# Performance work log

Measured on AMD Instinct MI355X. Metric: run time of the kernel, lower is better.

The kernel has to match this reference:

```python
import jax, jax.numpy as jnp
import numpy as np

D = 256          # input_size
RNN = 256        # rnn_hidden
COND = 64        # cond_dim
HID = 128        # MLP hidden
N_FIXED = 128    # mask.sum() with alternating mask
N_FREE = D - N_FIXED
B = 131072

# Static index arrays implementing the boolean mask (even indices fixed).
IDX_FIXED = np.arange(0, D, 2)
IDX_FREE = np.arange(1, D, 2)


def setup_inputs() -> dict:
    key = jax.random.key(0)
    ks = jax.random.split(key, 8)
    in_dim = N_FIXED + RNN + COND  # 448
    x = jax.random.normal(ks[0], (B, D), jnp.float32)
    h = jax.random.normal(ks[1], (B, RNN + COND), jnp.float32)
    W1 = jax.random.normal(ks[2], (in_dim, HID), jnp.float32) / np.sqrt(in_dim)
    b1 = jnp.zeros((HID,), jnp.float32)
    W2 = jax.random.normal(ks[3], (HID, HID), jnp.float32) / np.sqrt(HID)
    b2 = jnp.zeros((HID,), jnp.float32)
    W3 = jax.random.normal(ks[4], (HID, N_FREE * 2), jnp.float32) / np.sqrt(HID)
    b3 = jnp.zeros((N_FREE * 2,), jnp.float32)
    return {"x": x, "h": h, "W1": W1, "b1": b1, "W2": W2, "b2": b2, "W3": W3, "b3": b3}


def reference(x, h, W1, b1, W2, b2, W3, b3):
    # gather fixed / free halves (static index gather == boolean-mask select)
    x_fixed = x[:, IDX_FIXED]          # [B, N_FIXED]
    x_free = x[:, IDX_FREE]            # [B, N_FREE]
    z = jnp.concatenate([x_fixed, h], axis=-1)  # [B, 448]
    a = jax.nn.relu(z @ W1 + b1)
    a = jax.nn.relu(a @ W2 + b2)
    st = a @ W3 + b3                   # [B, 2*N_FREE]
    s = jnp.tanh(st[:, :N_FREE])
    t = st[:, N_FREE:]
    y_free = x_free * jnp.exp(s) + t
    log_det = jnp.sum(s, axis=-1)
    # scatter-write back into output layout
    y = jnp.zeros_like(x).at[:, IDX_FIXED].set(x_fixed).at[:, IDX_FREE].set(y_free)
    return y, log_det
```

## Files before the change

kernel.cpp:

```cpp
#include <hip/hip_runtime.h>
#include <stdint.h>

typedef __attribute__((ext_vector_type(8))) short bf16x8;
typedef __attribute__((ext_vector_type(4))) float f32x4;

#define B_ROWS 131072
#define BM 32
#define ZP 456
#define AP 136

#define Z_OFF    0
#define Z_BYTES  (BM * ZP * 2)
#define A1_OFF   (Z_OFF + Z_BYTES)
#define A1_BYTES (BM * AP * 2)
#define BIAS_OFF (A1_OFF + A1_BYTES)
#define BIAS_BYTES (512 * 4)
#define LDET_OFF (BIAS_OFF + BIAS_BYTES)
#define LDS_TOTAL (LDET_OFF + 4 * BM * 4)

#define W1P_OFF 0
#define W2P_OFF 7168
#define W3P_OFF 9216

__device__ inline uint16_t f2bf(float x) {
  uint32_t u = __float_as_uint(x);
  u += 0x7fffu + ((u >> 16) & 1u);
  return (uint16_t)(u >> 16);
}

__device__ inline float tanh_fast(float x) {
  x = fminf(fmaxf(x, -15.f), 15.f);
  float e = __expf(2.f * x);
  return (e - 1.f) / (e + 1.f);
}

__global__ void prepack_kernel(const float* __restrict__ W1,
                               const float* __restrict__ W2,
                               const float* __restrict__ W3,
                               uint4* __restrict__ wp) {
  int tid = blockIdx.x * 256 + threadIdx.x;
  if (tid >= 13312) return;
  int l = tid & 63, f = tid >> 6;
  const float* W; int N, kt, nt;
  if (f < 112)      { W = W1; N = 128; int ff = f;       nt = ff / 14; kt = ff - nt * 14; }
  else if (f < 144) { W = W2; N = 128; int ff = f - 112; nt = ff >> 2; kt = ff & 3; }
  else              { W = W3; N = 256; int ff = f - 144; nt = ff >> 2; kt = ff & 3; }
  int k0  = kt * 32 + (l >> 4) * 8;
  int col = nt * 16 + (l & 15);
  uint16_t v[8];
#pragma unroll
  for (int j = 0; j < 8; j++) v[j] = f2bf(W[(size_t)(k0 + j) * N + col]);
  uint4 o;
  o.x = (uint32_t)v[0] | ((uint32_t)v[1] << 16);
  o.y = (uint32_t)v[2] | ((uint32_t)v[3] << 16);
  o.z = (uint32_t)v[4] | ((uint32_t)v[5] << 16);
  o.w = (uint32_t)v[6] | ((uint32_t)v[7] << 16);
  wp[tid] = o;
}

__global__ __launch_bounds__(256, 4) void fused_kernel(
    const float* __restrict__ x, const float* __restrict__ h,
    const float* __restrict__ b1, const float* __restrict__ b2,
    const float* __restrict__ b3, const uint4* __restrict__ wp,
    float* __restrict__ y, float* __restrict__ ldet) {
  extern __shared__ uint8_t smem[];
  uint16_t* zs  = (uint16_t*)(smem + Z_OFF);
  uint16_t* a1  = (uint16_t*)(smem + A1_OFF);
  uint16_t* a2  = (uint16_t*)(smem + Z_OFF);
  float*    bias = (float*)(smem + BIAS_OFF);
  float*    lsum = (float*)(smem + LDET_OFF);

  const int t  = threadIdx.x;
  const int m0 = blockIdx.x * BM;

  for (int i = t; i < 512; i += 256)
    bias[i] = (i < 128) ? b1[i] : (i < 256) ? b2[i - 128] : b3[i - 256];

  {
    const float4* xg = (const float4*)(x + (size_t)m0 * 256);
#pragma unroll
    for (int k = 0; k < 8; k++) {
      int idx = t + k * 256;
      int row = idx >> 6, c4 = idx & 63;
      float4 v = xg[idx];
      uint32_t p = (uint32_t)f2bf(v.x) | ((uint32_t)f2bf(v.z) << 16);
      *(uint32_t*)&zs[row * ZP + c4 * 2] = p;
    }
    const float4* hg = (const float4*)(h + (size_t)m0 * 320);
#pragma unroll
    for (int k = 0; k < 10; k++) {
      int idx = t + k * 256;
      int row = idx / 80, c4 = idx - row * 80;
      float4 v = hg[idx];
      uint2 p;
      p.x = (uint32_t)f2bf(v.x) | ((uint32_t)f2bf(v.y) << 16);
      p.y = (uint32_t)f2bf(v.z) | ((uint32_t)f2bf(v.w) << 16);
      *(uint2*)&zs[row * ZP + 128 + c4 * 4] = p;
    }
  }
  __syncthreads();

  const int wid = t >> 6, l = t & 63;
  const int lr = l & 15, lq = l >> 4;

  {
    f32x4 acc[2][2] = {};
#pragma unroll 2
    for (int kt = 0; kt < 14; kt++) {
      bf16x8 afr[2];
#pragma unroll
      for (int mi = 0; mi < 2; mi++)
        afr[mi] = *(const bf16x8*)&zs[(mi * 16 + lr) * ZP + kt * 32 + lq * 8];
      bf16x8 bfr[2];
#pragma unroll
      for (int nj = 0; nj < 2; nj++)
        bfr[nj] = *(const bf16x8*)&wp[W1P_OFF + ((wid * 2 + nj) * 14 + kt) * 64 + l];
#pragma unroll
      for (int mi = 0; mi < 2; mi++)
#pragma unroll
        for (int nj = 0; nj < 2; nj++)
          acc[mi][nj] = __builtin_amdgcn_mfma_f32_16x16x32_bf16(afr[mi], bfr[nj], acc[mi][nj], 0, 0, 0);
    }
#pragma unroll
    for (int mi = 0; mi < 2; mi++)
#pragma unroll
      for (int nj = 0; nj < 2; nj++) {
        int col = wid * 32 + nj * 16 + lr;
        float bv = bias[col];
#pragma unroll
        for (int r = 0; r < 4; r++) {
          int row = mi * 16 + lq * 4 + r;
          a1[row * AP + col] = f2bf(fmaxf(acc[mi][nj][r] + bv, 0.f));
        }
      }
  }
  __syncthreads();

  {
    f32x4 acc[2][2] = {};
#pragma unroll
    for (int kt = 0; kt < 4; kt++) {
      bf16x8 afr[2];
#pragma unroll
      for (int mi = 0; mi < 2; mi++)
        afr[mi] = *(const bf16x8*)&a1[(mi * 16 + lr) * AP + kt * 32 + lq * 8];
      bf16x8 bfr[2];
#pragma unroll
      for (int nj = 0; nj < 2; nj++)
        bfr[nj] = *(const bf16x8*)&wp[W2P_OFF + ((wid * 2 + nj) * 4 + kt) * 64 + l];
#pragma unroll
      for (int mi = 0; mi < 2; mi++)
#pragma unroll
        for (int nj = 0; nj < 2; nj++)
          acc[mi][nj] = __builtin_amdgcn_mfma_f32_16x16x32_bf16(afr[mi], bfr[nj], acc[mi][nj], 0, 0, 0);
    }
    __syncthreads();
#pragma unroll
    for (int mi = 0; mi < 2; mi++)
#pragma unroll
      for (int nj = 0; nj < 2; nj++) {
        int col = wid * 32 + nj * 16 + lr;
        float bv = bias[128 + col];
#pragma unroll
        for (int r = 0; r < 4; r++) {
          int row = mi * 16 + lq * 4 + r;
          a2[row * AP + col] = f2bf(fmaxf(acc[mi][nj][r] + bv, 0.f));
        }
      }
  }
  __syncthreads();

  float2 xv[2][2][4];
#pragma unroll
  for (int mi = 0; mi < 2; mi++)
#pragma unroll
    for (int nj = 0; nj < 2; nj++) {
      int colc = wid * 32 + nj * 16 + lr;
#pragma unroll
      for (int r = 0; r < 4; r++) {
        int grow = m0 + mi * 16 + lq * 4 + r;
        xv[mi][nj][r] = *(const float2*)(x + (size_t)grow * 256 + 2 * colc);
      }
    }

  f32x4 acc3[2][4] = {};
#pragma unroll
  for (int kt = 0; kt < 4; kt++) {
    bf16x8 afr[2];
#pragma unroll
    for (int mi = 0; mi < 2; mi++)
      afr[mi] = *(const bf16x8*)&a2[(mi * 16 + lr) * AP + kt * 32 + lq * 8];
    bf16x8 bfr[4];
#pragma unroll
    for (int nj = 0; nj < 2; nj++) {
      bfr[nj]     = *(const bf16x8*)&wp[W3P_OFF + ((wid * 2 + nj) * 4 + kt) * 64 + l];
      bfr[nj + 2] = *(const bf16x8*)&wp[W3P_OFF + ((8 + wid * 2 + nj) * 4 + kt) * 64 + l];
    }
#pragma unroll
    for (int mi = 0; mi < 2; mi++)
#pragma unroll
      for (int nj = 0; nj < 4; nj++)
        acc3[mi][nj] = __builtin_amdgcn_mfma_f32_16x16x32_bf16(afr[mi], bfr[nj], acc3[mi][nj], 0, 0, 0);
  }

  float lp[2][4];
#pragma unroll
  for (int mi = 0; mi < 2; mi++)
#pragma unroll
    for (int r = 0; r < 4; r++) lp[mi][r] = 0.f;

#pragma unroll
  for (int mi = 0; mi < 2; mi++) {
#pragma unroll
    for (int nj = 0; nj < 2; nj++) {
      int colc = wid * 32 + nj * 16 + lr;
      float bs = bias[256 + colc];
      float bt = bias[384 + colc];
#pragma unroll
      for (int r = 0; r < 4; r++) {
        int grow = m0 + mi * 16 + lq * 4 + r;
        float sv = tanh_fast(acc3[mi][nj][r] + bs);
        float tv = acc3[mi][nj + 2][r] + bt;
        lp[mi][r] += sv;
        float2 o;
        o.x = xv[mi][nj][r].x;
        o.y = xv[mi][nj][r].y * __expf(sv) + tv;
        *(float2*)(y + (size_t)grow * 256 + 2 * colc) = o;
      }
    }
  }

#pragma unroll
  for (int mi = 0; mi < 2; mi++)
#pragma unroll
    for (int r = 0; r < 4; r++) {
      float v = lp[mi][r];
      v += __shfl_xor(v, 1);
      v += __shfl_xor(v, 2);
      v += __shfl_xor(v, 4);
      v += __shfl_xor(v, 8);
      if (lr == 0) lsum[wid * BM + mi * 16 + lq * 4 + r] = v;
    }
  __syncthreads();
  if (t < BM) ldet[m0 + t] = lsum[t] + lsum[BM + t] + lsum[2 * BM + t] + lsum[3 * BM + t];
}

extern "C" void kernel_launch(void* const* d_in, const int* in_sizes, int n_in,
                              void* d_out, int out_size, void* d_ws, size_t ws_size,
                              hipStream_t stream) {
  const float* x  = (const float*)d_in[0];
  const float* h  = (const float*)d_in[1];
  const float* W1 = (const float*)d_in[2];
  const float* b1 = (const float*)d_in[3];
  const float* W2 = (const float*)d_in[4];
  const float* b2 = (const float*)d_in[5];
  const float* W3 = (const float*)d_in[6];
  const float* b3 = (const float*)d_in[7];
  float* y    = (float*)d_out;
  float* ldet = y + (size_t)B_ROWS * 256;
  uint4* wp   = (uint4*)d_ws;

  prepack_kernel<<<52, 256, 0, stream>>>(W1, W2, W3, wp);

  hipFuncSetAttribute((const void*)fused_kernel,
                      hipFuncAttributeMaxDynamicSharedMemorySize, LDS_TOTAL);
  fused_kernel<<<B_ROWS / BM, 256, LDS_TOTAL, stream>>>(x, h, b1, b2, b3, wp, y, ldet);
}
```

Measured before the change: 122.7 us.

## Make fused kernel persistent with double-buffered register prefetch of next tile

Switches from one 32-row tile per block to 512 persistent blocks that each process 8 tiles. The next tile's x and h rows are loaded into registers while the current tile's MLP runs, then written to a second LDS buffer, which aims to hide global load latency behind MFMA work. Launch bounds drop to 2 blocks per CU to make room for the extra registers and the doubled Z buffer. This lowers occupancy, and with 512 blocks on a 256-CU part the per-CU parallelism is small.

```diff
diff --git a/kernel.cpp b/kernel.cpp
--- a/kernel.cpp
+++ b/kernel.cpp
@@ -6,16 +6,15 @@
 
 #define B_ROWS 131072
 #define BM 32
+#define NT 8
+#define GRID 512
 #define ZP 456
 #define AP 136
 
-#define Z_OFF    0
-#define Z_BYTES  (BM * ZP * 2)
-#define A1_OFF   (Z_OFF + Z_BYTES)
-#define A1_BYTES (BM * AP * 2)
-#define BIAS_OFF (A1_OFF + A1_BYTES)
-#define BIAS_BYTES (512 * 4)
-#define LDET_OFF (BIAS_OFF + BIAS_BYTES)
+#define ZBYTES   (BM * ZP * 2)
+#define A1_OFF   (2 * ZBYTES)
+#define BIAS_OFF (A1_OFF + BM * AP * 2)
+#define LDET_OFF (BIAS_OFF + 512 * 4)
 #define LDS_TOTAL (LDET_OFF + 4 * BM * 4)
 
 #define W1P_OFF 0
@@ -58,191 +57,214 @@
   wp[tid] = o;
 }
 
-__global__ __launch_bounds__(256, 4) void fused_kernel(
+__device__ inline void stage_write(uint16_t* zn, int t,
+                                   const float4* xr, const float4* hr) {
+#pragma unroll
+  for (int k = 0; k < 8; k++) {
+    int idx = t + k * 256;
+    int row = idx >> 6, c4 = idx & 63;
+    uint32_t p = (uint32_t)f2bf(xr[k].x) | ((uint32_t)f2bf(xr[k].z) << 16);
+    *(uint32_t*)&zn[row * ZP + c4 * 2] = p;
+  }
+#pragma unroll
+  for (int k = 0; k < 10; k++) {
+    int idx = t + k * 256;
+    int row = idx / 80, c4 = idx - row * 80;
+    uint2 p;
+    p.x = (uint32_t)f2bf(hr[k].x) | ((uint32_t)f2bf(hr[k].y) << 16);
+    p.y = (uint32_t)f2bf(hr[k].z) | ((uint32_t)f2bf(hr[k].w) << 16);
+    *(uint2*)&zn[row * ZP + 128 + c4 * 4] = p;
+  }
+}
+
+__global__ __launch_bounds__(256, 2) void fused_kernel(
     const float* __restrict__ x, const float* __restrict__ h,
     const float* __restrict__ b1, const float* __restrict__ b2,
     const float* __restrict__ b3, const uint4* __restrict__ wp,
     float* __restrict__ y, float* __restrict__ ldet) {
   extern __shared__ uint8_t smem[];
-  uint16_t* zs  = (uint16_t*)(smem + Z_OFF);
-  uint16_t* a1  = (uint16_t*)(smem + A1_OFF);
-  uint16_t* a2  = (uint16_t*)(smem + Z_OFF);
+  uint16_t* a1   = (uint16_t*)(smem + A1_OFF);
   float*    bias = (float*)(smem + BIAS_OFF);
   float*    lsum = (float*)(smem + LDET_OFF);
 
-  const int t  = threadIdx.x;
-  const int m0 = blockIdx.x * BM;
+  const int t = threadIdx.x;
+  const int wid = t >> 6, l = t & 63;
+  const int lr = l & 15, lq = l >> 4;
+  const int tile0 = blockIdx.x * NT;
 
   for (int i = t; i < 512; i += 256)
     bias[i] = (i < 128) ? b1[i] : (i < 256) ? b2[i - 128] : b3[i - 256];
 
   {
+    const int m0 = tile0 * BM;
+    float4 xr[8], hr[10];
     const float4* xg = (const float4*)(x + (size_t)m0 * 256);
 #pragma unroll
-    for (int k = 0; k < 8; k++) {
-      int idx = t + k * 256;
-      int row = idx >> 6, c4 = idx & 63;
-      float4 v = xg[idx];
-      uint32_t p = (uint32_t)f2bf(v.x) | ((uint32_t)f2bf(v.z) << 16);
-      *(uint32_t*)&zs[row * ZP + c4 * 2] = p;
-    }
+    for (int k = 0; k < 8; k++) xr[k] = xg[t + k * 256];
     const float4* hg = (const float4*)(h + (size_t)m0 * 320);
 #pragma unroll
-    for (int k = 0; k < 10; k++) {
-      int idx = t + k * 256;
-      int row = idx / 80, c4 = idx - row * 80;
-      float4 v = hg[idx];
-      uint2 p;
-      p.x = (uint32_t)f2bf(v.x) | ((uint32_t)f2bf(v.y) << 16);
-      p.y = (uint32_t)f2bf(v.z) | ((uint32_t)f2bf(v.w) << 16);
-      *(uint2*)&zs[row * ZP + 128 + c4 * 4] = p;
-    }
+    for (int k = 0; k < 10; k++) hr[k] = hg[t + k * 256];
+    stage_write((uint16_t*)smem, t, xr, hr);
   }
   __syncthreads();
 
-  const int wid = t >> 6, l = t & 63;
-  const int lr = l & 15, lq = l >> 4;
-
-  {
-    f32x4 acc[2][2] = {};
+  int cur = 0;
+  for (int it = 0; it < NT; ++it) {
+    const int m0 = (tile0 + it) * BM;
+    uint16_t* zc = (uint16_t*)(smem + cur * ZBYTES);
+    uint16_t* zn = (uint16_t*)(smem + (cur ^ 1) * ZBYTES);
+    uint16_t* a2 = zc;
+
+    float4 xr[8], hr[10];
+    const bool pf = (it + 1 < NT);
+    if (pf) {
+      const float4* xg = (const float4*)(x + (size_t)(m0 + BM) * 256);
+#pragma unroll
+      for (int k = 0; k < 8; k++) xr[k] = xg[t + k * 256];
+      const float4* hg = (const float4*)(h + (size_t)(m0 + BM) * 320);
+#pragma unroll
+      for (int k = 0; k < 10; k++) hr[k] = hg[t + k * 256];
+    }
+
+    {
+      f32x4 acc[2][2] = {};
 #pragma unroll 2
-    for (int kt = 0; kt < 14; kt++) {
-      bf16x8 afr[2];
-#pragma unroll
-      for (int mi = 0; mi < 2; mi++)
-        afr[mi] = *(const bf16x8*)&zs[(mi * 16 + lr) * ZP + kt * 32 + lq * 8];
-      bf16x8 bfr[2];
-#pragma unroll
-      for (int nj = 0; nj < 2; nj++)
-        bfr[nj] = *(const bf16x8*)&wp[W1P_OFF + ((wid * 2 + nj) * 14 + kt) * 64 + l];
-#pragma unroll
-      for (int mi = 0; mi < 2; mi++)
+      for (int kt = 0; kt < 14; kt++) {
+        bf16x8 afr[2];
+#pragma unroll
+        for (int mi = 0; mi < 2; mi++)
+          afr[mi] = *(const bf16x8*)&zc[(mi * 16 + lr) * ZP + kt * 32 + lq * 8];
+        bf16x8 bfr[2];
 #pragma unroll
         for (int nj = 0; nj < 2; nj++)
-          acc[mi][nj] = __builtin_amdgcn_mfma_f32_16x16x32_bf16(afr[mi], bfr[nj], acc[mi][nj], 0, 0, 0);
-    }
+          bfr[nj] = *(const bf16x8*)&wp[W1P_OFF + ((wid * 2 + nj) * 14 + kt) * 64 + l];
+#pragma unroll
+        for (int mi = 0; mi < 2; mi++)
+#pragma unroll
+          for (int nj = 0; nj < 2; nj++)
+            acc[mi][nj] = __builtin_amdgcn_mfma_f32_16x16x32_bf16(afr[mi], bfr[nj], acc[mi][nj], 0, 0, 0);
+      }
+#pragma unroll
+      for (int mi = 0; mi < 2; mi++)
+#pragma unroll
+        for (int nj = 0; nj < 2; nj++) {
+          int col = wid * 32 + nj * 16 + lr;
+          float bv = bias[col];
+#pragma unroll
+          for (int r = 0; r < 4; r++)
+            a1[(mi * 16 + lq * 4 + r) * AP + col] = f2bf(fmaxf(acc[mi][nj][r] + bv, 0.f));
+        }
+    }
+    __syncthreads();
+
+    {
+      f32x4 acc[2][2] = {};
+#pragma unroll
+      for (int kt = 0; kt < 4; kt++) {
+        bf16x8 afr[2];
+#pragma unroll
+        for (int mi = 0; mi < 2; mi++)
+          afr[mi] = *(const bf16x8*)&a1[(mi * 16 + lr) * AP + kt * 32 + lq * 8];
+        bf16x8 bfr[2];
+#pragma unroll
+        for (int nj = 0; nj < 2; nj++)
+          bfr[nj] = *(const bf16x8*)&wp[W2P_OFF + ((wid * 2 + nj) * 4 + kt) * 64 + l];
+#pragma unroll
+        for (int mi = 0; mi < 2; mi++)
+#pragma unroll
+          for (int nj = 0; nj < 2; nj++)
+            acc[mi][nj] = __builtin_amdgcn_mfma_f32_16x16x32_bf16(afr[mi], bfr[nj], acc[mi][nj], 0, 0, 0);
+      }
+#pragma unroll
+      for (int mi = 0; mi < 2; mi++)
+#pragma unroll
+        for (int nj = 0; nj < 2; nj++) {
+          int col = wid * 32 + nj * 16 + lr;
+          float bv = bias[128 + col];
+#pragma unroll
+          for (int r = 0; r < 4; r++)
+            a2[(mi * 16 + lq * 4 + r) * AP + col] = f2bf(fmaxf(acc[mi][nj][r] + bv, 0.f));
+        }
+    }
+    __syncthreads();
+
+    float2 xv[2][2][4];
 #pragma unroll
     for (int mi = 0; mi < 2; mi++)
 #pragma unroll
       for (int nj = 0; nj < 2; nj++) {
-        int col = wid * 32 + nj * 16 + lr;
-        float bv = bias[col];
+        int colc = wid * 32 + nj * 16 + lr;
 #pragma unroll
         for (int r = 0; r < 4; r++) {
-          int row = mi * 16 + lq * 4 + r;
-          a1[row * AP + col] = f2bf(fmaxf(acc[mi][nj][r] + bv, 0.f));
-        }
-      }
-  }
-  __syncthreads();
-
-  {
-    f32x4 acc[2][2] = {};
+          int grow = m0 + mi * 16 + lq * 4 + r;
+          xv[mi][nj][r] = *(const float2*)(x + (size_t)grow * 256 + 2 * colc);
+        }
+      }
+
+    f32x4 acc3[2][4] = {};
 #pragma unroll
     for (int kt = 0; kt < 4; kt++) {
       bf16x8 afr[2];
 #pragma unroll
       for (int mi = 0; mi < 2; mi++)
-        afr[mi] = *(const bf16x8*)&a1[(mi * 16 + lr) * AP + kt * 32 + lq * 8];
-      bf16x8 bfr[2];
-#pragma unroll
-      for (int nj = 0; nj < 2; nj++)
-        bfr[nj] = *(const bf16x8*)&wp[W2P_OFF + ((wid * 2 + nj) * 4 + kt) * 64 + l];
-#pragma unroll
-      for (int mi = 0; mi < 2; mi++)
-#pragma unroll
-        for (int nj = 0; nj < 2; nj++)
-          acc[mi][nj] = __builtin_amdgcn_mfma_f32_16x16x32_bf16(afr[mi], bfr[nj], acc[mi][nj], 0, 0, 0);
-    }
-    __syncthreads();
-#pragma unroll
-    for (int mi = 0; mi < 2; mi++)
+        afr[mi] = *(const bf16x8*)&a2[(mi * 16 + lr) * AP + kt * 32 + lq * 8];
+      bf16x8 bfr[4];
 #pragma unroll
       for (int nj = 0; nj < 2; nj++) {
-        int col = wid * 32 + nj * 16 + lr;
-        float bv = bias[128 + col];
+        bfr[nj]     = *(const bf16x8*)&wp[W3P_OFF + ((wid * 2 + nj) * 4 + kt) * 64 + l];
+        bfr[nj + 2] = *(const bf16x8*)&wp[W3P_OFF + ((8 + wid * 2 + nj) * 4 + kt) * 64 + l];
+      }
+#pragma unroll
+      for (int mi = 0; mi < 2; mi++)
+#pragma unroll
+        for (int nj = 0; nj < 4; nj++)
+          acc3[mi][nj] = __builtin_amdgcn_mfma_f32_16x16x32_bf16(afr[mi], bfr[nj], acc3[mi][nj], 0, 0, 0);
+    }
+
+    float lp[2][4];
+#pragma unroll
+    for (int mi = 0; mi < 2; mi++)
+#pragma unroll
+      for (int r = 0; r < 4; r++) lp[mi][r] = 0.f;
+
+#pragma unroll
+    for (int mi = 0; mi < 2; mi++)
+#pragma unroll
+      for (int nj = 0; nj < 2; nj++) {
+        int colc = wid * 32 + nj * 16 + lr;
+        float bs = bias[256 + colc];
+        float bt = bias[384 + colc];
 #pragma unroll
         for (int r = 0; r < 4; r++) {
-          int row = mi * 16 + lq * 4 + r;
-          a2[row * AP + col] = f2bf(fmaxf(acc[mi][nj][r] + bv, 0.f));
-        }
-      }
-  }
-  __syncthreads();
-
-  float2 xv[2][2][4];
-#pragma unroll
-  for (int mi = 0; mi < 2; mi++)
-#pragma unroll
-    for (int nj = 0; nj < 2; nj++) {
-      int colc = wid * 32 + nj * 16 + lr;
+          int grow = m0 + mi * 16 + lq * 4 + r;
+          float sv = tanh_fast(acc3[mi][nj][r] + bs);
+          float tv = acc3[mi][nj + 2][r] + bt;
+          lp[mi][r] += sv;
+          float2 o;
+          o.x = xv[mi][nj][r].x;
+          o.y = xv[mi][nj][r].y * __expf(sv) + tv;
+          *(float2*)(y + (size_t)grow * 256 + 2 * colc) = o;
+        }
+      }
+
+#pragma unroll
+    for (int mi = 0; mi < 2; mi++)
 #pragma unroll
       for (int r = 0; r < 4; r++) {
-        int grow = m0 + mi * 16 + lq * 4 + r;
-        xv[mi][nj][r] = *(const float2*)(x + (size_t)grow * 256 + 2 * colc);
-      }
-    }
-
-  f32x4 acc3[2][4] = {};
-#pragma unroll
-  for (int kt = 0; kt < 4; kt++) {
-    bf16x8 afr[2];
-#pragma unroll
-    for (int mi = 0; mi < 2; mi++)
-      afr[mi] = *(const bf16x8*)&a2[(mi * 16 + lr) * AP + kt * 32 + lq * 8];
-    bf16x8 bfr[4];
-#pragma unroll
-    for (int nj = 0; nj < 2; nj++) {
-      bfr[nj]     = *(const bf16x8*)&wp[W3P_OFF + ((wid * 2 + nj) * 4 + kt) * 64 + l];
-      bfr[nj + 2] = *(const bf16x8*)&wp[W3P_OFF + ((8 + wid * 2 + nj) * 4 + kt) * 64 + l];
-    }
-#pragma unroll
-    for (int mi = 0; mi < 2; mi++)
-#pragma unroll
-      for (int nj = 0; nj < 4; nj++)
-        acc3[mi][nj] = __builtin_amdgcn_mfma_f32_16x16x32_bf16(afr[mi], bfr[nj], acc3[mi][nj], 0, 0, 0);
-  }
-
-  float lp[2][4];
-#pragma unroll
-  for (int mi = 0; mi < 2; mi++)
-#pragma unroll
-    for (int r = 0; r < 4; r++) lp[mi][r] = 0.f;
-
-#pragma unroll
-  for (int mi = 0; mi < 2; mi++) {
-#pragma unroll
-    for (int nj = 0; nj < 2; nj++) {
-      int colc = wid * 32 + nj * 16 + lr;
-      float bs = bias[256 + colc];
-      float bt = bias[384 + colc];
-#pragma unroll
-      for (int r = 0; r < 4; r++) {
-        int grow = m0 + mi * 16 + lq * 4 + r;
-        float sv = tanh_fast(acc3[mi][nj][r] + bs);
-        float tv = acc3[mi][nj + 2][r] + bt;
-        lp[mi][r] += sv;
-        float2 o;
-        o.x = xv[mi][nj][r].x;
-        o.y = xv[mi][nj][r].y * __expf(sv) + tv;
-        *(float2*)(y + (size_t)grow * 256 + 2 * colc) = o;
-      }
-    }
-  }
-
-#pragma unroll
-  for (int mi = 0; mi < 2; mi++)
-#pragma unroll
-    for (int r = 0; r < 4; r++) {
-      float v = lp[mi][r];
-      v += __shfl_xor(v, 1);
-      v += __shfl_xor(v, 2);
-      v += __shfl_xor(v, 4);
-      v += __shfl_xor(v, 8);
-      if (lr == 0) lsum[wid * BM + mi * 16 + lq * 4 + r] = v;
-    }
-  __syncthreads();
-  if (t < BM) ldet[m0 + t] = lsum[t] + lsum[BM + t] + lsum[2 * BM + t] + lsum[3 * BM + t];
+        float v = lp[mi][r];
+        v += __shfl_xor(v, 1);
+        v += __shfl_xor(v, 2);
+        v += __shfl_xor(v, 4);
+        v += __shfl_xor(v, 8);
+        if (lr == 0) lsum[wid * BM + mi * 16 + lq * 4 + r] = v;
+      }
+    __syncthreads();
+    if (t < BM) ldet[m0 + t] = lsum[t] + lsum[BM + t] + lsum[2 * BM + t] + lsum[3 * BM + t];
+
+    if (pf) stage_write(zn, t, xr, hr);
+    __syncthreads();
+    cur ^= 1;
+  }
 }
 
 extern "C" void kernel_launch(void* const* d_in, const int* in_sizes, int n_in,
@@ -262,7 +284,7 @@
 
   prepack_kernel<<<52, 256, 0, stream>>>(W1, W2, W3, wp);
 
-  hipFuncSetAttribute((const void*)fused_kernel,
-                      hipFuncAttributeMaxDynamicSharedMemorySize, LDS_TOTAL);
-  fused_kernel<<<B_ROWS / BM, 256, LDS_TOTAL, stream>>>(x, h, b1, b2, b3, wp, y, ldet);
-}
+  (void)hipFuncSetAttribute((const void*)fused_kernel,
+                            hipFuncAttributeMaxDynamicSharedMemorySize, LDS_TOTAL);
+  fused_kernel<<<GRID, 256, LDS_TOTAL, stream>>>(x, h, b1, b2, b3, wp, y, ldet);
+}
```

New measurement: 238.9 us. 94.6% more time.
